# Optimization experiments

Measured on AMD Instinct MI355X. Metric: run time of the kernel, lower is better.

The kernel has to match this reference:

```python
import jax, jax.numpy as jnp
import numpy as np

N = 50000
E = 800000
IN_DIM = 128
HID = 64
HEADS = 4
NUM_CLASSES = 40
NEG_SLOPE = 0.2
BN_EPS = 1e-5
SM_EPS = 1e-16


def setup_inputs() -> dict:
    key = jax.random.key(0)
    ks = jax.random.split(key, 12)
    d1 = HID * HEADS
    s_in = 1.0 / np.sqrt(IN_DIM)
    s_d1 = 1.0 / np.sqrt(d1)
    return {
        "x": jax.random.normal(ks[0], (N, IN_DIM), dtype=jnp.float32),
        "edge_index": jax.random.randint(ks[1], (2, E), 0, N, dtype=jnp.int32),
        # layer 1 (heads=4, concat)
        "Wl1": jax.random.normal(ks[2], (IN_DIM, d1), dtype=jnp.float32) * s_in,
        "Wr1": jax.random.normal(ks[3], (IN_DIM, d1), dtype=jnp.float32) * s_in,
        "att1": jax.random.normal(ks[4], (HEADS, HID), dtype=jnp.float32) * (1.0 / np.sqrt(HID)),
        "b1": jnp.zeros((d1,), dtype=jnp.float32),
        "gamma1": jnp.ones((d1,), dtype=jnp.float32),
        "beta1": jnp.zeros((d1,), dtype=jnp.float32),
        # layer 2 (heads=1, mean)
        "Wl2": jax.random.normal(ks[5], (d1, NUM_CLASSES), dtype=jnp.float32) * s_d1,
        "Wr2": jax.random.normal(ks[6], (d1, NUM_CLASSES), dtype=jnp.float32) * s_d1,
        "att2": jax.random.normal(ks[7], (1, NUM_CLASSES), dtype=jnp.float32) * (1.0 / np.sqrt(NUM_CLASSES)),
        "b2": jnp.zeros((NUM_CLASSES,), dtype=jnp.float32),
    }


def _gatv2_conv(x, Wl, Wr, att, b, src, dst, heads, out_ch, concat):
    n = x.shape[0]
    xl = (x @ Wl).reshape(n, heads, out_ch)   # source transform
    xr = (x @ Wr).reshape(n, heads, out_ch)   # target transform
    # per-edge attention logits (GATv2): a^T LeakyReLU(xl_j + xr_i)
    s = xl[src] + xr[dst]                                    # [E, H, C]
    e = jnp.einsum('ehc,hc->eh', jax.nn.leaky_relu(s, NEG_SLOPE), att)  # [E, H]
    # segment softmax over incoming edges of each dst node
    m = jax.ops.segment_max(e, dst, num_segments=n)          # [N, H]
    a = jnp.exp(e - m[dst])
    denom = jax.ops.segment_sum(a, dst, num_segments=n)
    alpha = a / (denom[dst] + SM_EPS)                        # [E, H]
    # aggregate messages alpha * xl_j
    out = jax.ops.segment_sum(alpha[..., None] * xl[src], dst, num_segments=n)  # [N, H, C]
    out = out.reshape(n, heads * out_ch) if concat else out.mean(axis=1)
    return out + b


def _batchnorm(h, gamma, beta):
    mu = h.mean(axis=0)
    var = h.var(axis=0)
    return gamma * (h - mu) * jax.lax.rsqrt(var + BN_EPS) + beta


def reference(x, edge_index, Wl1, Wr1, att1, b1, gamma1, beta1, Wl2, Wr2, att2, b2):
    n = x.shape[0]
    # add self-loops (PyG GATv2Conv default add_self_loops=True)
    loop = jnp.arange(n, dtype=edge_index.dtype)
    src = jnp.concatenate([edge_index[0], loop])
    dst = jnp.concatenate([edge_index[1], loop])
    h = _gatv2_conv(x, Wl1, Wr1, att1, b1, src, dst, HEADS, HID, True)
    h = jax.nn.elu(_batchnorm(h, gamma1, beta1))
    # eval mode: dropout is identity
    return _gatv2_conv(h, Wl2, Wr2, att2, b2, src, dst, 1, NUM_CLASSES, False)
```

## Files before the change

kernel.cpp:

```cpp
#include <hip/hip_runtime.h>
#include <math.h>

#define N_NODES 50000
#define N_EDGES 800000
#define ET (N_EDGES + N_NODES)
#define IN_DIM 128
#define HID 64
#define HEADS 4
#define D1 256
#define NCLS 40
#define NEG_SLOPE 0.2f
#define BN_EPS 1e-5f
#define SM_EPS 1e-16f
#define NB 196

typedef unsigned short ushort_t;
typedef __attribute__((ext_vector_type(8))) short short8;
typedef __attribute__((ext_vector_type(16))) float f32x16;

__device__ __forceinline__ float eluf(float x) { return x > 0.f ? x : expm1f(x); }
__device__ __forceinline__ float lrelu(float x) { return x >= 0.f ? x : NEG_SLOPE * x; }
__device__ __forceinline__ unsigned short f2bf(float f) {
    unsigned int u = __float_as_uint(f);
    u += 0x7fffu + ((u >> 16) & 1u);
    return (unsigned short)(u >> 16);
}
__device__ __forceinline__ float bf2f(ushort_t u) {
    return __uint_as_float(((unsigned int)u) << 16);
}

__global__ void k_deg(const int* __restrict__ ei, int* __restrict__ deg) {
    int e = blockIdx.x * blockDim.x + threadIdx.x;
    if (e >= ET) return;
    int dst = (e < N_EDGES) ? ei[N_EDGES + e] : (e - N_EDGES);
    atomicAdd(&deg[dst], 1);
}

__global__ __launch_bounds__(256) void k_scan1(const int* __restrict__ deg,
                                               int* __restrict__ row_st,
                                               int* __restrict__ bsum) {
    __shared__ int wsum[4], woff[4];
    const int t = threadIdx.x, w = t >> 6, lane = t & 63;
    const int idx = blockIdx.x * 256 + t;
    int v = (idx < N_NODES) ? deg[idx] : 0;
    int s = v;
    #pragma unroll
    for (int off = 1; off < 64; off <<= 1) {
        int y = __shfl_up(s, off, 64);
        if (lane >= off) s += y;
    }
    if (lane == 63) wsum[w] = s;
    __syncthreads();
    if (t == 0) {
        int run = 0;
        #pragma unroll
        for (int i2 = 0; i2 < 4; i2++) { woff[i2] = run; run += wsum[i2]; }
        bsum[blockIdx.x] = run;
    }
    __syncthreads();
    if (idx < N_NODES) row_st[idx] = woff[w] + (s - v);
}

__global__ __launch_bounds__(256) void k_scan2(int* __restrict__ bsum) {
    __shared__ int wsum[4], woff[4];
    const int t = threadIdx.x, w = t >> 6, lane = t & 63;
    int v = (t < NB) ? bsum[t] : 0;
    int s = v;
    #pragma unroll
    for (int off = 1; off < 64; off <<= 1) {
        int y = __shfl_up(s, off, 64);
        if (lane >= off) s += y;
    }
    if (lane == 63) wsum[w] = s;
    __syncthreads();
    if (t == 0) {
        int run = 0;
        #pragma unroll
        for (int i2 = 0; i2 < 4; i2++) { woff[i2] = run; run += wsum[i2]; }
    }
    __syncthreads();
    if (t < NB) bsum[t] = woff[w] + (s - v);
}

__global__ void k_scan3(int* __restrict__ row_st, int* __restrict__ cursor,
                        const int* __restrict__ bsum) {
    const int idx = blockIdx.x * 256 + threadIdx.x;
    if (idx < N_NODES) {
        int r = row_st[idx] + bsum[blockIdx.x];
        row_st[idx] = r;
        cursor[idx] = r;
    }
    if (idx == 0) row_st[N_NODES] = ET;
}

__global__ void k_scatter(const int* __restrict__ ei, int* __restrict__ cursor,
                          int* __restrict__ csr_src) {
    int e = blockIdx.x * blockDim.x + threadIdx.x;
    if (e >= ET) return;
    int src, dst;
    if (e < N_EDGES) { src = ei[e]; dst = ei[N_EDGES + e]; }
    else             { src = dst = e - N_EDGES; }
    int pos = atomicAdd(&cursor[dst], 1);
    csr_src[pos] = src;
}

__global__ void k_cvt_x(const float* __restrict__ x, ushort_t* __restrict__ xb, int n4) {
    int i = blockIdx.x * blockDim.x + threadIdx.x;
    if (i >= n4) return;
    float4 v = ((const float4*)x)[i];
    ushort4 o;
    o.x = f2bf(v.x); o.y = f2bf(v.y); o.z = f2bf(v.z); o.w = f2bf(v.w);
    ((ushort4*)xb)[i] = o;
}

__global__ void k_cvt_w1(const float* __restrict__ Wl, const float* __restrict__ Wr,
                         ushort_t* __restrict__ BT) {
    int n = blockIdx.x;
    int k = threadIdx.x;
    float v = (n < 256) ? Wl[k * 256 + n] : Wr[k * 256 + (n - 256)];
    BT[n * 128 + k] = f2bf(v);
}

__global__ void k_cvt_w2(const float* __restrict__ Wl, const float* __restrict__ Wr,
                         ushort_t* __restrict__ BT) {
    int n = blockIdx.x;
    int k = threadIdx.x;
    float v = 0.f;
    if (n < 40)      v = Wl[k * 40 + n];
    else if (n < 80) v = Wr[k * 40 + (n - 40)];
    BT[n * 256 + k] = f2bf(v);
}

#define MBM 128
#define MBN 128
#define MBK 64
template<typename OT>
__global__ __launch_bounds__(256) void k_mgemm(
    const ushort_t* __restrict__ A, const ushort_t* __restrict__ BT,
    OT* __restrict__ C, int M, int K, int N, int ldc)
{
    __shared__ __align__(16) ushort_t Al[MBM * MBK];
    __shared__ __align__(16) ushort_t Bl[MBN * MBK];
    const int t = threadIdx.x;
    const int w = t >> 6, L = t & 63;
    const int i0 = blockIdx.x * MBM;
    const int j0 = blockIdx.y * MBN;
    const int wm = (w >> 1) * 64, wn = (w & 1) * 64;
    const int l31 = L & 31, half = L >> 5;

    int sm[4], sca[4];
    #pragma unroll
    for (int r = 0; r < 4; r++) {
        int s = (r * 4 + w) * 64 + L;
        int m = s >> 3;
        sm[r] = m;
        sca[r] = (s & 7) ^ (m & 7);
    }

    f32x16 acc[2][2];
    #pragma unroll
    for (int a = 0; a < 2; a++)
        #pragma unroll
        for (int b = 0; b < 2; b++)
            #pragma unroll
            for (int r = 0; r < 16; r++) acc[a][b][r] = 0.f;

    for (int kt = 0; kt < K; kt += MBK) {
        short8 sa[4], sb[4];
        #pragma unroll
        for (int r = 0; r < 4; r++) {
            int row = i0 + sm[r]; if (row >= M) row = M - 1;
            sa[r] = *(const short8*)&A[(size_t)row * K + kt + sca[r] * 8];
            sb[r] = *(const short8*)&BT[(size_t)(j0 + sm[r]) * K + kt + sca[r] * 8];
        }
        __syncthreads();
        #pragma unroll
        for (int r = 0; r < 4; r++) {
            int s = (r * 4 + w) * 64 + L;
            *(short8*)&Al[s * 8] = sa[r];
            *(short8*)&Bl[s * 8] = sb[r];
        }
        __syncthreads();
        #pragma unroll
        for (int ks = 0; ks < 4; ks++) {
            short8 af[2], bfr[2];
            #pragma unroll
            for (int mt = 0; mt < 2; mt++) {
                int m = wm + mt * 32 + l31;
                int c = (ks * 2 + half) ^ (m & 7);
                af[mt] = *(const short8*)&Al[(m * 8 + c) * 8];
            }
            #pragma unroll
            for (int nt = 0; nt < 2; nt++) {
                int n = wn + nt * 32 + l31;
                int c = (ks * 2 + half) ^ (n & 7);
                bfr[nt] = *(const short8*)&Bl[(n * 8 + c) * 8];
            }
            #pragma unroll
            for (int mt = 0; mt < 2; mt++)
                #pragma unroll
                for (int nt = 0; nt < 2; nt++)
                    acc[mt][nt] = __builtin_amdgcn_mfma_f32_32x32x16_bf16(
                        af[mt], bfr[nt], acc[mt][nt], 0, 0, 0);
        }
    }
    #pragma unroll
    for (int mt = 0; mt < 2; mt++)
        #pragma unroll
        for (int nt = 0; nt < 2; nt++) {
            int col = j0 + wn + nt * 32 + l31;
            int rbase = i0 + wm + mt * 32 + 4 * half;
            if (col < N) {
                #pragma unroll
                for (int r = 0; r < 16; r++) {
                    int row = rbase + (r & 3) + 8 * (r >> 2);
                    if (row < M) {
                        if constexpr (sizeof(OT) == 2)
                            C[(size_t)row * ldc + col] = (OT)f2bf(acc[mt][nt][r]);
                        else
                            C[(size_t)row * ldc + col] = acc[mt][nt][r];
                    }
                }
            }
        }
}

__global__ __launch_bounds__(256) void k_mgemm_bn(
    const float* __restrict__ A, const ushort_t* __restrict__ BT,
    ushort_t* __restrict__ C, int M, int K, int N, int ldc,
    const float* __restrict__ bn_g, const float* __restrict__ bn_b)
{
    __shared__ __align__(16) ushort_t Al[MBM * MBK];
    __shared__ __align__(16) ushort_t Bl[MBN * MBK];
    __shared__ float gsh[256], bsh[256];
    const int t = threadIdx.x;
    const int w = t >> 6, L = t & 63;
    const int i0 = blockIdx.x * MBM;
    const int j0 = blockIdx.y * MBN;
    const int wm = (w >> 1) * 64, wn = (w & 1) * 64;
    const int l31 = L & 31, half = L >> 5;
    gsh[t] = bn_g[t]; bsh[t] = bn_b[t];
    __syncthreads();

    int sm[4], sca[4];
    #pragma unroll
    for (int r = 0; r < 4; r++) {
        int s = (r * 4 + w) * 64 + L;
        int m = s >> 3;
        sm[r] = m;
        sca[r] = (s & 7) ^ (m & 7);
    }

    f32x16 acc[2][2];
    #pragma unroll
    for (int a = 0; a < 2; a++)
        #pragma unroll
        for (int b = 0; b < 2; b++)
            #pragma unroll
            for (int r = 0; r < 16; r++) acc[a][b][r] = 0.f;

    for (int kt = 0; kt < K; kt += MBK) {
        short8 sa[4], sb[4];
        #pragma unroll
        for (int r = 0; r < 4; r++) {
            int row = i0 + sm[r]; if (row >= M) row = M - 1;
            int kb = kt + sca[r] * 8;
            float4 v0 = *(const float4*)&A[(size_t)row * K + kb];
            float4 v1 = *(const float4*)&A[(size_t)row * K + kb + 4];
            float4 g0 = *(const float4*)&gsh[kb];
            float4 g1 = *(const float4*)&gsh[kb + 4];
            float4 b0 = *(const float4*)&bsh[kb];
            float4 b1v = *(const float4*)&bsh[kb + 4];
            short8 o;
            o[0] = (short)f2bf(eluf(g0.x * v0.x + b0.x));
            o[1] = (short)f2bf(eluf(g0.y * v0.y + b0.y));
            o[2] = (short)f2bf(eluf(g0.z * v0.z + b0.z));
            o[3] = (short)f2bf(eluf(g0.w * v0.w + b0.w));
            o[4] = (short)f2bf(eluf(g1.x * v1.x + b1v.x));
            o[5] = (short)f2bf(eluf(g1.y * v1.y + b1v.y));
            o[6] = (short)f2bf(eluf(g1.z * v1.z + b1v.z));
            o[7] = (short)f2bf(eluf(g1.w * v1.w + b1v.w));
            sa[r] = o;
            sb[r] = *(const short8*)&BT[(size_t)(j0 + sm[r]) * K + kb];
        }
        __syncthreads();
        #pragma unroll
        for (int r = 0; r < 4; r++) {
            int s = (r * 4 + w) * 64 + L;
            *(short8*)&Al[s * 8] = sa[r];
            *(short8*)&Bl[s * 8] = sb[r];
        }
        __syncthreads();
        #pragma unroll
        for (int ks = 0; ks < 4; ks++) {
            short8 af[2], bfr[2];
            #pragma unroll
            for (int mt = 0; mt < 2; mt++) {
                int m = wm + mt * 32 + l31;
                int c = (ks * 2 + half) ^ (m & 7);
                af[mt] = *(const short8*)&Al[(m * 8 + c) * 8];
            }
            #pragma unroll
            for (int nt = 0; nt < 2; nt++) {
                int n = wn + nt * 32 + l31;
                int c = (ks * 2 + half) ^ (n & 7);
                bfr[nt] = *(const short8*)&Bl[(n * 8 + c) * 8];
            }
            #pragma unroll
            for (int mt = 0; mt < 2; mt++)
                #pragma unroll
                for (int nt = 0; nt < 2; nt++)
                    acc[mt][nt] = __builtin_amdgcn_mfma_f32_32x32x16_bf16(
                        af[mt], bfr[nt], acc[mt][nt], 0, 0, 0);
        }
    }
    #pragma unroll
    for (int mt = 0; mt < 2; mt++)
        #pragma unroll
        for (int nt = 0; nt < 2; nt++) {
            int col = j0 + wn + nt * 32 + l31;
            int rbase = i0 + wm + mt * 32 + 4 * half;
            if (col < N) {
                #pragma unroll
                for (int r = 0; r < 16; r++) {
                    int row = rbase + (r & 3) + 8 * (r >> 2);
                    if (row < M)
                        C[(size_t)row * ldc + col] = f2bf(acc[mt][nt][r]);
                }
            }
        }
}

#define CH1 16
#define XLS 260
__global__ __launch_bounds__(256) void k_node1(
    const ushort_t* __restrict__ xlr, const int* __restrict__ row_start,
    const int* __restrict__ csr_src, const float* __restrict__ att1,
    const float* __restrict__ b1, float* __restrict__ h1)
{
    __shared__ __align__(16) float xl_sh[CH1 * XLS];
    __shared__ __align__(16) float p_sh[HEADS][CH1];
    const int i = blockIdx.x;
    const int t = threadIdx.x;
    const int h = t >> 6, lane = t & 63;
    const int qe = lane >> 2, qq = lane & 3;
    const int half = lane >> 5, l31 = lane & 31;
    const int s0 = row_start[i], s1 = row_start[i + 1];

    float xr_t[16], at_t[16];
    {
        const ushort_t* xrp = &xlr[(size_t)i * 512 + 256 + h * 64 + qq * 16];
        const float* atp = &att1[h * 64 + qq * 16];
        #pragma unroll
        for (int k = 0; k < 16; k += 4) {
            ushort4 u = *(const ushort4*)&xrp[k];
            float4 b = *(const float4*)&atp[k];
            xr_t[k + 0] = bf2f(u.x); xr_t[k + 1] = bf2f(u.y);
            xr_t[k + 2] = bf2f(u.z); xr_t[k + 3] = bf2f(u.w);
            at_t[k + 0] = b.x; at_t[k + 1] = b.y; at_t[k + 2] = b.z; at_t[k + 3] = b.w;
        }
    }
    const float bvv = b1[t];

    float acc = 0.f, l_run = 0.f;

    int base = s0;
    const int nfull = (s1 - s0) >> 4;
    for (int f = 0; f < nfull; f++, base += CH1) {
        __syncthreads();
        #pragma unroll
        for (int r = 0; r < 2; r++) {
            int e = r * 8 + h * 2 + half;
            int src = csr_src[base + e];
            const ushort_t* gp = &xlr[(size_t)src * 512];
            ushort4 u0 = *(const ushort4*)&gp[4 * l31];
            ushort4 u1 = *(const ushort4*)&gp[128 + 4 * l31];
            float4 f0 = make_float4(bf2f(u0.x), bf2f(u0.y), bf2f(u0.z), bf2f(u0.w));
            float4 f1 = make_float4(bf2f(u1.x), bf2f(u1.y), bf2f(u1.z), bf2f(u1.w));
            *(float4*)&xl_sh[e * XLS + 4 * l31] = f0;
            *(float4*)&xl_sh[e * XLS + 128 + 4 * l31] = f1;
        }
        __syncthreads();
        float dot = 0.f;
        {
            const float* xp = &xl_sh[qe * XLS + h * 64 + qq * 16];
            #pragma unroll
            for (int k = 0; k < 16; k += 4) {
                float4 v = *(const float4*)&xp[k];
                dot += lrelu(v.x + xr_t[k + 0]) * at_t[k + 0];
                dot += lrelu(v.y + xr_t[k + 1]) * at_t[k + 1];
                dot += lrelu(v.z + xr_t[k + 2]) * at_t[k + 2];
                dot += lrelu(v.w + xr_t[k + 3]) * at_t[k + 3];
            }
        }
        dot += __shfl_xor(dot, 1, 64);
        dot += __shfl_xor(dot, 2, 64);
        if (qq == 0) p_sh[h][qe] = __expf(dot);
        float4 P0 = *(const float4*)&p_sh[h][0];
        float4 P1 = *(const float4*)&p_sh[h][4];
        float4 P2 = *(const float4*)&p_sh[h][8];
        float4 P3 = *(const float4*)&p_sh[h][12];
        float p[16] = {P0.x, P0.y, P0.z, P0.w, P1.x, P1.y, P1.z, P1.w,
                       P2.x, P2.y, P2.z, P2.w, P3.x, P3.y, P3.z, P3.w};
        float lsum = 0.f;
        #pragma unroll
        for (int e = 0; e < 16; e++) lsum += p[e];
        l_run += lsum;
        #pragma unroll
        for (int e = 0; e < 16; e++)
            acc += p[e] * xl_sh[e * XLS + t];
    }
    const int rem = s1 - base;
    if (rem > 0) {
        __syncthreads();
        #pragma unroll
        for (int r = 0; r < 2; r++) {
            int e = r * 8 + h * 2 + half;
            if (e < rem) {
                int src = csr_src[base + e];
                const ushort_t* gp = &xlr[(size_t)src * 512];
                ushort4 u0 = *(const ushort4*)&gp[4 * l31];
                ushort4 u1 = *(const ushort4*)&gp[128 + 4 * l31];
                float4 f0 = make_float4(bf2f(u0.x), bf2f(u0.y), bf2f(u0.z), bf2f(u0.w));
                float4 f1 = make_float4(bf2f(u1.x), bf2f(u1.y), bf2f(u1.z), bf2f(u1.w));
                *(float4*)&xl_sh[e * XLS + 4 * l31] = f0;
                *(float4*)&xl_sh[e * XLS + 128 + 4 * l31] = f1;
            }
        }
        __syncthreads();
        float dot = 0.f;
        {
            const float* xp = &xl_sh[qe * XLS + h * 64 + qq * 16];
            #pragma unroll
            for (int k = 0; k < 16; k += 4) {
                float4 v = *(const float4*)&xp[k];
                dot += lrelu(v.x + xr_t[k + 0]) * at_t[k + 0];
                dot += lrelu(v.y + xr_t[k + 1]) * at_t[k + 1];
                dot += lrelu(v.z + xr_t[k + 2]) * at_t[k + 2];
                dot += lrelu(v.w + xr_t[k + 3]) * at_t[k + 3];
            }
        }
        dot += __shfl_xor(dot, 1, 64);
        dot += __shfl_xor(dot, 2, 64);
        if (qq == 0) p_sh[h][qe] = (qe < rem) ? __expf(dot) : 0.f;
        for (int e = 0; e < rem; e++) {
            float pe = p_sh[h][e];
            l_run += pe;
            acc += pe * xl_sh[e * XLS + t];
        }
    }
    h1[(size_t)i * 256 + t] = acc / (l_run + SM_EPS) + bvv;
}

__global__ void k_bnstats(const float* __restrict__ h1, float* __restrict__ bn_sum,
                          float* __restrict__ bn_sumsq) {
    const int t = threadIdx.x;
    const int rows_per = (N_NODES + gridDim.x - 1) / gridDim.x;
    const int r0 = blockIdx.x * rows_per;
    const int r1 = min(N_NODES, r0 + rows_per);
    float s = 0.f, s2 = 0.f;
    for (int r = r0; r < r1; r++) {
        float v = h1[(size_t)r * 256 + t];
        s += v; s2 += v * v;
    }
    atomicAdd(&bn_sum[t], s);
    atomicAdd(&bn_sumsq[t], s2);
}

__global__ void k_bnfinal(const float* __restrict__ bn_sum, const float* __restrict__ bn_sumsq,
                          const float* __restrict__ gamma, const float* __restrict__ beta,
                          float* __restrict__ bn_g, float* __restrict__ bn_b) {
    const int t = threadIdx.x;
    float mean = bn_sum[t] * (1.f / N_NODES);
    float var = bn_sumsq[t] * (1.f / N_NODES) - mean * mean;
    float g = gamma[t] * rsqrtf(var + BN_EPS);
    bn_g[t] = g;
    bn_b[t] = beta[t] - g * mean;
}

#define C2S 44
__global__ __launch_bounds__(256) void k_node2(
    const ushort_t* __restrict__ xlr2, const int* __restrict__ row_start,
    const int* __restrict__ csr_src, const float* __restrict__ att2,
    const float* __restrict__ b2, float* __restrict__ out)
{
    __shared__ __align__(16) float xl_sh[4][16 * C2S];
    __shared__ __align__(16) float p_sh[4][16];
    __shared__ int src_sh[4][16];
    const int wv = threadIdx.x >> 6, L = threadIdx.x & 63;
    const int i = blockIdx.x * 4 + wv;
    const int qe = L >> 2, qq = L & 3;
    const bool node_ok = (i < N_NODES);
    int s0 = 0, s1 = 0;
    if (node_ok) { s0 = row_start[i]; s1 = row_start[i + 1]; }
    float at_t[10], xr_t[10];
    #pragma unroll
    for (int r = 0; r < 10; r++) at_t[r] = att2[qq + 4 * r];
    if (node_ok) {
        const ushort_t* xrp = &xlr2[(size_t)i * 80 + 40];
        #pragma unroll
        for (int r = 0; r < 10; r++) xr_t[r] = bf2f(xrp[qq + 4 * r]);
    }

    float accv = 0.f, l_run = 0.f;
    const int cagg = (L < NCLS) ? L : 0;
    const int e16 = L & 15, k16 = L >> 4;

    if (node_ok) {
        int base = s0;
        const int nfull = (s1 - s0) >> 4;
        for (int f = 0; f < nfull; f++, base += 16) {
            if (L < 16) src_sh[wv][L] = csr_src[base + L];
            {
                short8 u = *(const short8*)&xlr2[(size_t)src_sh[wv][e16] * 80 + k16 * 8];
                float4 f0 = make_float4(bf2f((ushort_t)u[0]), bf2f((ushort_t)u[1]),
                                        bf2f((ushort_t)u[2]), bf2f((ushort_t)u[3]));
                float4 f1 = make_float4(bf2f((ushort_t)u[4]), bf2f((ushort_t)u[5]),
                                        bf2f((ushort_t)u[6]), bf2f((ushort_t)u[7]));
                *(float4*)&xl_sh[wv][e16 * C2S + k16 * 8] = f0;
                *(float4*)&xl_sh[wv][e16 * C2S + k16 * 8 + 4] = f1;
                if (L < 16) {
                    short8 u2 = *(const short8*)&xlr2[(size_t)src_sh[wv][L] * 80 + 32];
                    float4 g0 = make_float4(bf2f((ushort_t)u2[0]), bf2f((ushort_t)u2[1]),
                                            bf2f((ushort_t)u2[2]), bf2f((ushort_t)u2[3]));
                    float4 g1 = make_float4(bf2f((ushort_t)u2[4]), bf2f((ushort_t)u2[5]),
                                            bf2f((ushort_t)u2[6]), bf2f((ushort_t)u2[7]));
                    *(float4*)&xl_sh[wv][L * C2S + 32] = g0;
                    *(float4*)&xl_sh[wv][L * C2S + 36] = g1;
                }
            }
            float dot = 0.f;
            #pragma unroll
            for (int r = 0; r < 10; r++) {
                float v = xl_sh[wv][qe * C2S + qq + 4 * r];
                dot += lrelu(v + xr_t[r]) * at_t[r];
            }
            dot += __shfl_xor(dot, 1, 64);
            dot += __shfl_xor(dot, 2, 64);
            if (qq == 0) p_sh[wv][qe] = __expf(dot);
            float4 P0 = *(const float4*)&p_sh[wv][0];
            float4 P1 = *(const float4*)&p_sh[wv][4];
            float4 P2 = *(const float4*)&p_sh[wv][8];
            float4 P3 = *(const float4*)&p_sh[wv][12];
            float p[16] = {P0.x, P0.y, P0.z, P0.w, P1.x, P1.y, P1.z, P1.w,
                           P2.x, P2.y, P2.z, P2.w, P3.x, P3.y, P3.z, P3.w};
            float lsum = 0.f;
            #pragma unroll
            for (int e = 0; e < 16; e++) lsum += p[e];
            l_run += lsum;
            #pragma unroll
            for (int e = 0; e < 16; e++)
                accv += p[e] * xl_sh[wv][e * C2S + cagg];
        }
        const int rem = s1 - base;
        if (rem > 0) {
            if (L < rem) src_sh[wv][L] = csr_src[base + L];
            if (e16 < rem) {
                short8 u = *(const short8*)&xlr2[(size_t)src_sh[wv][e16] * 80 + k16 * 8];
                float4 f0 = make_float4(bf2f((ushort_t)u[0]), bf2f((ushort_t)u[1]),
                                        bf2f((ushort_t)u[2]), bf2f((ushort_t)u[3]));
                float4 f1 = make_float4(bf2f((ushort_t)u[4]), bf2f((ushort_t)u[5]),
                                        bf2f((ushort_t)u[6]), bf2f((ushort_t)u[7]));
                *(float4*)&xl_sh[wv][e16 * C2S + k16 * 8] = f0;
                *(float4*)&xl_sh[wv][e16 * C2S + k16 * 8 + 4] = f1;
            }
            if (L < rem) {
                short8 u2 = *(const short8*)&xlr2[(size_t)src_sh[wv][L] * 80 + 32];
                float4 g0 = make_float4(bf2f((ushort_t)u2[0]), bf2f((ushort_t)u2[1]),
                                        bf2f((ushort_t)u2[2]), bf2f((ushort_t)u2[3]));
                float4 g1 = make_float4(bf2f((ushort_t)u2[4]), bf2f((ushort_t)u2[5]),
                                        bf2f((ushort_t)u2[6]), bf2f((ushort_t)u2[7]));
                *(float4*)&xl_sh[wv][L * C2S + 32] = g0;
                *(float4*)&xl_sh[wv][L * C2S + 36] = g1;
            }
            float dot = 0.f;
            #pragma unroll
            for (int r = 0; r < 10; r++) {
                float v = xl_sh[wv][qe * C2S + qq + 4 * r];
                dot += lrelu(v + xr_t[r]) * at_t[r];
            }
            dot += __shfl_xor(dot, 1, 64);
            dot += __shfl_xor(dot, 2, 64);
            if (qq == 0) p_sh[wv][qe] = (qe < rem) ? __expf(dot) : 0.f;
            for (int e = 0; e < rem; e++) {
                float pe = p_sh[wv][e];
                l_run += pe;
                accv += pe * xl_sh[wv][e * C2S + cagg];
            }
        }
    }
    if (node_ok && L < NCLS)
        out[(size_t)i * 40 + L] = accv / (l_run + SM_EPS) + b2[L];
}

static inline size_t align_up(size_t v, size_t a) { return (v + a - 1) & ~(a - 1); }

extern "C" void kernel_launch(void* const* d_in, const int* in_sizes, int n_in,
                              void* d_out, int out_size, void* d_ws, size_t ws_size,
                              hipStream_t stream)
{
    const float* x     = (const float*)d_in[0];
    const int*   ei    = (const int*)d_in[1];
    const float* Wl1   = (const float*)d_in[2];
    const float* Wr1   = (const float*)d_in[3];
    const float* att1  = (const float*)d_in[4];
    const float* b1    = (const float*)d_in[5];
    const float* gamma1= (const float*)d_in[6];
    const float* beta1 = (const float*)d_in[7];
    const float* Wl2   = (const float*)d_in[8];
    const float* Wr2   = (const float*)d_in[9];
    const float* att2  = (const float*)d_in[10];
    const float* b2    = (const float*)d_in[11];
    float* out = (float*)d_out;

    char* ws = (char*)d_ws;
    size_t off = 0;
    ushort_t* xlr1b = (ushort_t*)(ws + off); off += (size_t)N_NODES * 512 * 2;
    float*    h1    = (float*)   (ws + off); off += (size_t)N_NODES * 256 * 4;
    int*   csr_src = (int*)  (ws + off); off += align_up((size_t)ET * 4, 256);
    int*   row_st  = (int*)  (ws + off); off += align_up((size_t)(N_NODES + 1) * 4, 256);
    int*   cursor  = (int*)  (ws + off); off += align_up((size_t)N_NODES * 4, 256);
    int*   deg     = (int*)  (ws + off); off += align_up((size_t)N_NODES * 4, 256);
    int*   bsum    = (int*)  (ws + off); off += align_up((size_t)NB * 4, 256);
    float* bn_sum  = (float*)(ws + off); off += 256 * 4;
    float* bn_sumsq= (float*)(ws + off); off += 256 * 4;
    float* bn_g    = (float*)(ws + off); off += 256 * 4;
    float* bn_b    = (float*)(ws + off); off += 256 * 4;
    ushort_t* BT1  = (ushort_t*)(ws + off); off += align_up((size_t)512 * 128 * 2, 256);
    ushort_t* BT2  = (ushort_t*)(ws + off); off += align_up((size_t)128 * 256 * 2, 256);
    ushort_t* xlr2b = xlr1b;
    ushort_t* xb    = (ushort_t*)h1;

    hipMemsetAsync(deg, 0, (size_t)N_NODES * 4, stream);
    hipMemsetAsync(bn_sum, 0, 512 * 4, stream);

    k_deg<<<(ET + 255) / 256, 256, 0, stream>>>(ei, deg);
    k_scan1<<<NB, 256, 0, stream>>>(deg, row_st, bsum);
    k_scan2<<<1, 256, 0, stream>>>(bsum);
    k_scan3<<<NB, 256, 0, stream>>>(row_st, cursor, bsum);
    k_scatter<<<(ET + 255) / 256, 256, 0, stream>>>(ei, cursor, csr_src);

    k_cvt_x<<<(N_NODES * IN_DIM / 4 + 255) / 256, 256, 0, stream>>>(x, xb, N_NODES * IN_DIM / 4);
    k_cvt_w1<<<512, 128, 0, stream>>>(Wl1, Wr1, BT1);
    k_cvt_w2<<<128, 256, 0, stream>>>(Wl2, Wr2, BT2);

    dim3 g1((N_NODES + MBM - 1) / MBM, 512 / MBN);
    k_mgemm<ushort_t><<<g1, 256, 0, stream>>>(xb, BT1, xlr1b, N_NODES, IN_DIM, 512, 512);
    k_node1<<<N_NODES, 256, 0, stream>>>(xlr1b, row_st, csr_src, att1, b1, h1);

    k_bnstats<<<1000, 256, 0, stream>>>(h1, bn_sum, bn_sumsq);
    k_bnfinal<<<1, 256, 0, stream>>>(bn_sum, bn_sumsq, gamma1, beta1, bn_g, bn_b);

    dim3 g2((N_NODES + MBM - 1) / MBM, 1);
    k_mgemm_bn<<<g2, 256, 0, stream>>>(h1, BT2, xlr2b, N_NODES, D1, 80, 80, bn_g, bn_b);
    k_node2<<<(N_NODES + 3) / 4, 256, 0, stream>>>(xlr2b, row_st, csr_src, att2, b2, out);
}
```

Before: 468.4 us.

## Fuse prep kernels, merge scan passes, fold BN finalize, prefetch CSR sources

Merges the degree count and the x/W1/W2 bf16 conversions into one multi-role launch. It removes the single-block scan2 by having each scan3 block sum the preceding block totals itself, and folds the BN finalize into the second GEMM's prologue. The two memsets become one. In k_node1 the next chunk's source indices are loaded early, overlapping that index fetch with compute. Together these cut kernel launches and serialized tiny kernels, at the cost of redundant bsum reads per block and the BN math being repeated in every GEMM block.

```diff
diff --git a/kernel.cpp b/kernel.cpp
--- a/kernel.cpp
+++ b/kernel.cpp
@@ -13,6 +13,8 @@
 #define BN_EPS 1e-5f
 #define SM_EPS 1e-16f
 #define NB 196
+#define DEGB 3321
+#define XB 6250
 
 typedef unsigned short ushort_t;
 typedef __attribute__((ext_vector_type(8))) short short8;
@@ -29,11 +31,40 @@
     return __uint_as_float(((unsigned int)u) << 16);
 }
 
-__global__ void k_deg(const int* __restrict__ ei, int* __restrict__ deg) {
-    int e = blockIdx.x * blockDim.x + threadIdx.x;
-    if (e >= ET) return;
-    int dst = (e < N_EDGES) ? ei[N_EDGES + e] : (e - N_EDGES);
-    atomicAdd(&deg[dst], 1);
+__global__ __launch_bounds__(256) void k_prep(
+    const int* __restrict__ ei, int* __restrict__ deg,
+    const float* __restrict__ x, ushort_t* __restrict__ xb,
+    const float* __restrict__ Wl1, const float* __restrict__ Wr1,
+    ushort_t* __restrict__ BT1,
+    const float* __restrict__ Wl2, const float* __restrict__ Wr2,
+    ushort_t* __restrict__ BT2)
+{
+    const int b = blockIdx.x, t = threadIdx.x;
+    if (b < DEGB) {
+        int e = b * 256 + t;
+        if (e < ET) {
+            int dst = (e < N_EDGES) ? ei[N_EDGES + e] : (e - N_EDGES);
+            atomicAdd(&deg[dst], 1);
+        }
+    } else if (b < DEGB + XB) {
+        int i = (b - DEGB) * 256 + t;
+        float4 v = ((const float4*)x)[i];
+        ushort4 o;
+        o.x = f2bf(v.x); o.y = f2bf(v.y); o.z = f2bf(v.z); o.w = f2bf(v.w);
+        ((ushort4*)xb)[i] = o;
+    } else if (b < DEGB + XB + 256) {
+        int n = (b - DEGB - XB) * 2 + (t >> 7);
+        int k = t & 127;
+        float v = (n < 256) ? Wl1[k * 256 + n] : Wr1[k * 256 + (n - 256)];
+        BT1[n * 128 + k] = f2bf(v);
+    } else {
+        int n = b - DEGB - XB - 256;
+        int k = t;
+        float v = 0.f;
+        if (n < 40)      v = Wl2[k * 40 + n];
+        else if (n < 80) v = Wr2[k * 40 + (n - 40)];
+        BT2[n * 256 + k] = f2bf(v);
+    }
 }
 
 __global__ __launch_bounds__(256) void k_scan1(const int* __restrict__ deg,
@@ -61,32 +92,21 @@
     if (idx < N_NODES) row_st[idx] = woff[w] + (s - v);
 }
 
-__global__ __launch_bounds__(256) void k_scan2(int* __restrict__ bsum) {
-    __shared__ int wsum[4], woff[4];
+__global__ __launch_bounds__(256) void k_scan3(int* __restrict__ row_st,
+                                               int* __restrict__ cursor,
+                                               const int* __restrict__ bsum) {
+    __shared__ int wred[4];
     const int t = threadIdx.x, w = t >> 6, lane = t & 63;
-    int v = (t < NB) ? bsum[t] : 0;
-    int s = v;
-    #pragma unroll
-    for (int off = 1; off < 64; off <<= 1) {
-        int y = __shfl_up(s, off, 64);
-        if (lane >= off) s += y;
-    }
-    if (lane == 63) wsum[w] = s;
+    int part = 0;
+    for (int j = t; j < blockIdx.x; j += 256) part += bsum[j];
+    #pragma unroll
+    for (int off = 32; off; off >>= 1) part += __shfl_xor(part, off, 64);
+    if (lane == 0) wred[w] = part;
     __syncthreads();
-    if (t == 0) {
-        int run = 0;
-        #pragma unroll
-        for (int i2 = 0; i2 < 4; i2++) { woff[i2] = run; run += wsum[i2]; }
-    }
-    __syncthreads();
-    if (t < NB) bsum[t] = woff[w] + (s - v);
-}
-
-__global__ void k_scan3(int* __restrict__ row_st, int* __restrict__ cursor,
-                        const int* __restrict__ bsum) {
-    const int idx = blockIdx.x * 256 + threadIdx.x;
+    const int pre = wred[0] + wred[1] + wred[2] + wred[3];
+    const int idx = blockIdx.x * 256 + t;
     if (idx < N_NODES) {
-        int r = row_st[idx] + bsum[blockIdx.x];
+        int r = row_st[idx] + pre;
         row_st[idx] = r;
         cursor[idx] = r;
     }
@@ -102,33 +122,6 @@
     else             { src = dst = e - N_EDGES; }
     int pos = atomicAdd(&cursor[dst], 1);
     csr_src[pos] = src;
-}
-
-__global__ void k_cvt_x(const float* __restrict__ x, ushort_t* __restrict__ xb, int n4) {
-    int i = blockIdx.x * blockDim.x + threadIdx.x;
-    if (i >= n4) return;
-    float4 v = ((const float4*)x)[i];
-    ushort4 o;
-    o.x = f2bf(v.x); o.y = f2bf(v.y); o.z = f2bf(v.z); o.w = f2bf(v.w);
-    ((ushort4*)xb)[i] = o;
-}
-
-__global__ void k_cvt_w1(const float* __restrict__ Wl, const float* __restrict__ Wr,
-                         ushort_t* __restrict__ BT) {
-    int n = blockIdx.x;
-    int k = threadIdx.x;
-    float v = (n < 256) ? Wl[k * 256 + n] : Wr[k * 256 + (n - 256)];
-    BT[n * 128 + k] = f2bf(v);
-}
-
-__global__ void k_cvt_w2(const float* __restrict__ Wl, const float* __restrict__ Wr,
-                         ushort_t* __restrict__ BT) {
-    int n = blockIdx.x;
-    int k = threadIdx.x;
-    float v = 0.f;
-    if (n < 40)      v = Wl[k * 40 + n];
-    else if (n < 80) v = Wr[k * 40 + (n - 40)];
-    BT[n * 256 + k] = f2bf(v);
 }
 
 #define MBM 128
@@ -228,7 +221,8 @@
 __global__ __launch_bounds__(256) void k_mgemm_bn(
     const float* __restrict__ A, const ushort_t* __restrict__ BT,
     ushort_t* __restrict__ C, int M, int K, int N, int ldc,
-    const float* __restrict__ bn_g, const float* __restrict__ bn_b)
+    const float* __restrict__ bn_sum, const float* __restrict__ bn_sumsq,
+    const float* __restrict__ gamma, const float* __restrict__ beta)
 {
     __shared__ __align__(16) ushort_t Al[MBM * MBK];
     __shared__ __align__(16) ushort_t Bl[MBN * MBK];
@@ -239,7 +233,13 @@
     const int j0 = blockIdx.y * MBN;
     const int wm = (w >> 1) * 64, wn = (w & 1) * 64;
     const int l31 = L & 31, half = L >> 5;
-    gsh[t] = bn_g[t]; bsh[t] = bn_b[t];
+    {
+        float mean = bn_sum[t] * (1.f / N_NODES);
+        float var = bn_sumsq[t] * (1.f / N_NODES) - mean * mean;
+        float g = gamma[t] * rsqrtf(var + BN_EPS);
+        gsh[t] = g;
+        bsh[t] = beta[t] - g * mean;
+    }
     __syncthreads();
 
     int sm[4], sca[4];
@@ -346,6 +346,7 @@
     const int qe = lane >> 2, qq = lane & 3;
     const int half = lane >> 5, l31 = lane & 31;
     const int s0 = row_start[i], s1 = row_start[i + 1];
+    const int e0 = h * 2 + half, e1 = 8 + h * 2 + half;
 
     float xr_t[16], at_t[16];
     {
@@ -366,21 +367,32 @@
 
     int base = s0;
     const int nfull = (s1 - s0) >> 4;
+    int src0 = csr_src[min(s0 + e0, s1 - 1)];
+    int src1 = csr_src[min(s0 + e1, s1 - 1)];
     for (int f = 0; f < nfull; f++, base += CH1) {
         __syncthreads();
-        #pragma unroll
-        for (int r = 0; r < 2; r++) {
-            int e = r * 8 + h * 2 + half;
-            int src = csr_src[base + e];
-            const ushort_t* gp = &xlr[(size_t)src * 512];
-            ushort4 u0 = *(const ushort4*)&gp[4 * l31];
-            ushort4 u1 = *(const ushort4*)&gp[128 + 4 * l31];
-            float4 f0 = make_float4(bf2f(u0.x), bf2f(u0.y), bf2f(u0.z), bf2f(u0.w));
-            float4 f1 = make_float4(bf2f(u1.x), bf2f(u1.y), bf2f(u1.z), bf2f(u1.w));
-            *(float4*)&xl_sh[e * XLS + 4 * l31] = f0;
-            *(float4*)&xl_sh[e * XLS + 128 + 4 * l31] = f1;
-        }
-        __syncthreads();
+        {
+            const ushort_t* gp0 = &xlr[(size_t)src0 * 512];
+            ushort4 a0 = *(const ushort4*)&gp0[4 * l31];
+            ushort4 a1 = *(const ushort4*)&gp0[128 + 4 * l31];
+            const ushort_t* gp1 = &xlr[(size_t)src1 * 512];
+            ushort4 c0 = *(const ushort4*)&gp1[4 * l31];
+            ushort4 c1 = *(const ushort4*)&gp1[128 + 4 * l31];
+            *(float4*)&xl_sh[e0 * XLS + 4 * l31] =
+                make_float4(bf2f(a0.x), bf2f(a0.y), bf2f(a0.z), bf2f(a0.w));
+            *(float4*)&xl_sh[e0 * XLS + 128 + 4 * l31] =
+                make_float4(bf2f(a1.x), bf2f(a1.y), bf2f(a1.z), bf2f(a1.w));
+            *(float4*)&xl_sh[e1 * XLS + 4 * l31] =
+                make_float4(bf2f(c0.x), bf2f(c0.y), bf2f(c0.z), bf2f(c0.w));
+            *(float4*)&xl_sh[e1 * XLS + 128 + 4 * l31] =
+                make_float4(bf2f(c1.x), bf2f(c1.y), bf2f(c1.z), bf2f(c1.w));
+        }
+        __syncthreads();
+        {
+            int nb = base + CH1;
+            src0 = csr_src[min(nb + e0, s1 - 1)];
+            src1 = csr_src[min(nb + e1, s1 - 1)];
+        }
         float dot = 0.f;
         {
             const float* xp = &xl_sh[qe * XLS + h * 64 + qq * 16];
@@ -413,19 +425,23 @@
     const int rem = s1 - base;
     if (rem > 0) {
         __syncthreads();
-        #pragma unroll
-        for (int r = 0; r < 2; r++) {
-            int e = r * 8 + h * 2 + half;
-            if (e < rem) {
-                int src = csr_src[base + e];
-                const ushort_t* gp = &xlr[(size_t)src * 512];
-                ushort4 u0 = *(const ushort4*)&gp[4 * l31];
-                ushort4 u1 = *(const ushort4*)&gp[128 + 4 * l31];
-                float4 f0 = make_float4(bf2f(u0.x), bf2f(u0.y), bf2f(u0.z), bf2f(u0.w));
-                float4 f1 = make_float4(bf2f(u1.x), bf2f(u1.y), bf2f(u1.z), bf2f(u1.w));
-                *(float4*)&xl_sh[e * XLS + 4 * l31] = f0;
-                *(float4*)&xl_sh[e * XLS + 128 + 4 * l31] = f1;
-            }
+        if (e0 < rem) {
+            const ushort_t* gp = &xlr[(size_t)src0 * 512];
+            ushort4 u0 = *(const ushort4*)&gp[4 * l31];
+            ushort4 u1 = *(const ushort4*)&gp[128 + 4 * l31];
+            *(float4*)&xl_sh[e0 * XLS + 4 * l31] =
+                make_float4(bf2f(u0.x), bf2f(u0.y), bf2f(u0.z), bf2f(u0.w));
+            *(float4*)&xl_sh[e0 * XLS + 128 + 4 * l31] =
+                make_float4(bf2f(u1.x), bf2f(u1.y), bf2f(u1.z), bf2f(u1.w));
+        }
+        if (e1 < rem) {
+            const ushort_t* gp = &xlr[(size_t)src1 * 512];
+            ushort4 u0 = *(const ushort4*)&gp[4 * l31];
+            ushort4 u1 = *(const ushort4*)&gp[128 + 4 * l31];
+            *(float4*)&xl_sh[e1 * XLS + 4 * l31] =
+                make_float4(bf2f(u0.x), bf2f(u0.y), bf2f(u0.z), bf2f(u0.w));
+            *(float4*)&xl_sh[e1 * XLS + 128 + 4 * l31] =
+                make_float4(bf2f(u1.x), bf2f(u1.y), bf2f(u1.z), bf2f(u1.w));
         }
         __syncthreads();
         float dot = 0.f;
@@ -465,17 +481,6 @@
     }
     atomicAdd(&bn_sum[t], s);
     atomicAdd(&bn_sumsq[t], s2);
-}
-
-__global__ void k_bnfinal(const float* __restrict__ bn_sum, const float* __restrict__ bn_sumsq,
-                          const float* __restrict__ gamma, const float* __restrict__ beta,
-                          float* __restrict__ bn_g, float* __restrict__ bn_b) {
-    const int t = threadIdx.x;
-    float mean = bn_sum[t] * (1.f / N_NODES);
-    float var = bn_sumsq[t] * (1.f / N_NODES) - mean * mean;
-    float g = gamma[t] * rsqrtf(var + BN_EPS);
-    bn_g[t] = g;
-    bn_b[t] = beta[t] - g * mean;
 }
 
 #define C2S 44
@@ -620,38 +625,33 @@
     int*   csr_src = (int*)  (ws + off); off += align_up((size_t)ET * 4, 256);
     int*   row_st  = (int*)  (ws + off); off += align_up((size_t)(N_NODES + 1) * 4, 256);
     int*   cursor  = (int*)  (ws + off); off += align_up((size_t)N_NODES * 4, 256);
+    int*   bsum    = (int*)  (ws + off); off += align_up((size_t)NB * 4, 256);
+    size_t zoff = off;
     int*   deg     = (int*)  (ws + off); off += align_up((size_t)N_NODES * 4, 256);
-    int*   bsum    = (int*)  (ws + off); off += align_up((size_t)NB * 4, 256);
     float* bn_sum  = (float*)(ws + off); off += 256 * 4;
     float* bn_sumsq= (float*)(ws + off); off += 256 * 4;
-    float* bn_g    = (float*)(ws + off); off += 256 * 4;
-    float* bn_b    = (float*)(ws + off); off += 256 * 4;
+    size_t zlen = off - zoff;
     ushort_t* BT1  = (ushort_t*)(ws + off); off += align_up((size_t)512 * 128 * 2, 256);
     ushort_t* BT2  = (ushort_t*)(ws + off); off += align_up((size_t)128 * 256 * 2, 256);
     ushort_t* xlr2b = xlr1b;
     ushort_t* xb    = (ushort_t*)h1;
 
-    hipMemsetAsync(deg, 0, (size_t)N_NODES * 4, stream);
-    hipMemsetAsync(bn_sum, 0, 512 * 4, stream);
-
-    k_deg<<<(ET + 255) / 256, 256, 0, stream>>>(ei, deg);
+    hipMemsetAsync(ws + zoff, 0, zlen, stream);
+
+    k_prep<<<DEGB + XB + 256 + 128, 256, 0, stream>>>(
+        ei, deg, x, xb, Wl1, Wr1, BT1, Wl2, Wr2, BT2);
     k_scan1<<<NB, 256, 0, stream>>>(deg, row_st, bsum);
-    k_scan2<<<1, 256, 0, stream>>>(bsum);
     k_scan3<<<NB, 256, 0, stream>>>(row_st, cursor, bsum);
-    k_scatter<<<(ET + 255) / 256, 256, 0, stream>>>(ei, cursor, csr_src);
-
-    k_cvt_x<<<(N_NODES * IN_DIM / 4 + 255) / 256, 256, 0, stream>>>(x, xb, N_NODES * IN_DIM / 4);
-    k_cvt_w1<<<512, 128, 0, stream>>>(Wl1, Wr1, BT1);
-    k_cvt_w2<<<128, 256, 0, stream>>>(Wl2, Wr2, BT2);
+    k_scatter<<<DEGB, 256, 0, stream>>>(ei, cursor, csr_src);
 
     dim3 g1((N_NODES + MBM - 1) / MBM, 512 / MBN);
     k_mgemm<ushort_t><<<g1, 256, 0, stream>>>(xb, BT1, xlr1b, N_NODES, IN_DIM, 512, 512);
     k_node1<<<N_NODES, 256, 0, stream>>>(xlr1b, row_st, csr_src, att1, b1, h1);
 
     k_bnstats<<<1000, 256, 0, stream>>>(h1, bn_sum, bn_sumsq);
-    k_bnfinal<<<1, 256, 0, stream>>>(bn_sum, bn_sumsq, gamma1, beta1, bn_g, bn_b);
 
     dim3 g2((N_NODES + MBM - 1) / MBM, 1);
-    k_mgemm_bn<<<g2, 256, 0, stream>>>(h1, BT2, xlr2b, N_NODES, D1, 80, 80, bn_g, bn_b);
+    k_mgemm_bn<<<g2, 256, 0, stream>>>(h1, BT2, xlr2b, N_NODES, D1, 80, 80,
+                                       bn_sum, bn_sumsq, gamma1, beta1);
     k_node2<<<(N_NODES + 3) / 4, 256, 0, stream>>>(xlr2b, row_st, csr_src, att2, b2, out);
 }
```

Result: faster. 428.7 us (-8.5%).
